# Performance work log

Measured on AMD Instinct MI355X. Metric: run time of the kernel, lower is better.

The kernel has to match this reference:

```python
import jax, jax.numpy as jnp
import numpy as np

B, T, D, E = 2, 1653, 512, 8
D_E = D // E
BE = B * E


def setup_inputs() -> dict:
    key = jax.random.key(0)
    ks = jax.random.split(key, 11)
    s = 0.02  # keep linear-layer scale sane
    return {
        "input": jax.random.normal(ks[0], (B, T, D), jnp.float32),
        "Wq": jax.random.normal(ks[1], (D, D), jnp.float32) * s,
        "bq": jax.random.normal(ks[2], (D,), jnp.float32) * s,
        "Wk": jax.random.normal(ks[3], (D, D), jnp.float32) * s,
        "bk": jax.random.normal(ks[4], (D,), jnp.float32) * s,
        "Wv": jax.random.normal(ks[5], (D, D), jnp.float32) * s,
        "bv": jax.random.normal(ks[6], (D,), jnp.float32) * s,
        "Wo": jax.random.normal(ks[7], (D, D), jnp.float32) * s,
        "bo": jax.random.normal(ks[8], (D,), jnp.float32) * s,
        # random 'gaussian orthogonal punishment' matrix (diag(norms) @ blockwise-QR in torch; random here)
        "punish": jax.random.normal(ks[9], (T, T), jnp.float32) * (1.0 / np.sqrt(T)),
        # random tensor produced by torch.nn.init.orthogonal_(att_score) in the source
        "att_orth": jax.random.normal(ks[10], (BE, T, T), jnp.float32) * (1.0 / np.sqrt(T)),
    }


def _learnable_sigmoid(x):
    return 1.2 / (1.0 + jnp.exp(-1.6 * x))


def reference(input, Wq, bq, Wk, bk, Wv, bv, Wo, bo, punish, att_orth):
    # torch nn.Linear: y = x @ W^T + b
    def proj(W, b):
        # [B,T,D] -> permute(0,2,1) -> [B,D,T] -> reshape to [B*E, T, D_E]
        y = jnp.einsum('btd,ed->bte', input, W) + b
        return y.transpose(0, 2, 1).reshape(BE, T, D_E)

    Q = _learnable_sigmoid(proj(Wq, bq))            # [BE, T, D_E] (mask_q is all-ones => no-op)
    K = _learnable_sigmoid(proj(Wk, bk))            # [BE, T, D_E]
    V = proj(Wv, bv)                                # [BE, T, D_E]

    inv_sqrt_T = 1.0 / jnp.sqrt(jnp.float32(T))
    att = jnp.einsum('btd,bsd->bts', Q, K) * inv_sqrt_T  # [BE, T, T]

    # punishment: elementwise mul by broadcast punish matrix, then matmul with
    # the (transposed) random orthogonal tensor: att = (att * P) @ orth^T
    att = (att * punish[None, :, :]) @ att_orth.transpose(0, 2, 1)  # [BE, T, T]

    att = jnp.where(att == 0.0, jnp.float32(-2e20), att)  # masked_fill(att==0, -2e20)

    out = jnp.einsum('bts,bsd->btd', att, V)        # [BE, T, D_E]
    # permute(0,2,1) -> [BE, D_E, T] -> reshape [B, D, T] -> permute -> [B, T, D]
    out = out.transpose(0, 2, 1).reshape(B, D, T).transpose(0, 2, 1)
    return jnp.einsum('btd,ed->bte', out, Wo) + bo   # [B, T, D]
```

## Files before the change

kernel.cpp:

```cpp
#include <hip/hip_runtime.h>

#define TT 1653
#define DD 512
#define BB 2
#define DE 64
#define BEH 16
#define TTILES 26
#define TPAD 1664
#define SQN 26
#define NJC 4
#define MPSTRIDE TPAD

typedef __attribute__((ext_vector_type(8))) short bf16x8;
typedef __attribute__((ext_vector_type(4))) float f32x4;
typedef float f32x4u  __attribute__((ext_vector_type(4), aligned(4)));

__device__ __forceinline__ short f2bf(float f) {
    union { float f; unsigned u; } v; v.f = f;
    unsigned r = v.u + 0x7fffu + ((v.u >> 16) & 1u);
    return (short)(r >> 16);
}
__device__ __forceinline__ unsigned pack2(float a, float b) {
    return (unsigned)(unsigned short)f2bf(a) | ((unsigned)(unsigned short)f2bf(b) << 16);
}
__device__ __forceinline__ float bf2f(short s) {
    union { unsigned u; float f; } v; v.u = ((unsigned)(unsigned short)s) << 16;
    return v.f;
}

__device__ __forceinline__ void bar_fenced() {
    __builtin_amdgcn_sched_barrier(0);
    __builtin_amdgcn_s_barrier();
    __builtin_amdgcn_sched_barrier(0);
}
__device__ __forceinline__ void lgkm0_bar() {
    asm volatile("s_waitcnt lgkmcnt(0)" ::: "memory");
    __builtin_amdgcn_sched_barrier(0);
    __builtin_amdgcn_s_barrier();
    __builtin_amdgcn_sched_barrier(0);
}

__global__ __launch_bounds__(256) void convp2_kernel(
    const float* __restrict__ P, short* __restrict__ Pbf)
{
    const int g = blockIdx.x * 256 + threadIdx.x;
    const int NG4 = TPAD / 4;
    if (g >= TT * NG4) return;
    const int r = g / NG4, c4 = (g - r * NG4) * 4;
    float p0 = 0.f, p1 = 0.f, p2 = 0.f, p3 = 0.f;
    const float* prow = P + (size_t)r * TT;
    if (c4 + 0 < TT) p0 = prow[c4 + 0];
    if (c4 + 1 < TT) p1 = prow[c4 + 1];
    if (c4 + 2 < TT) p2 = prow[c4 + 2];
    if (c4 + 3 < TT) p3 = prow[c4 + 3];
    uint2 o; o.x = pack2(p0, p1); o.y = pack2(p2, p3);
    *(uint2*)(Pbf + (size_t)r * TPAD + c4) = o;
}

__global__ __launch_bounds__(256) void proj4_kernel(
    const float* __restrict__ X,
    const float* __restrict__ W0, const float* __restrict__ b0,
    const float* __restrict__ W1, const float* __restrict__ b1,
    const float* __restrict__ W2, const float* __restrict__ b2,
    short* __restrict__ Y0, short* __restrict__ Y1, short* __restrict__ Y2)
{
    __shared__ __align__(16) short Wsh[64][72];
    __shared__ __align__(16) short Xs[64][72];

    const int tt = blockIdx.x, dt = blockIdx.y, z = blockIdx.z;
    const int b = z / 3, which = z % 3;
    const float* W    = (which == 0) ? W0 : (which == 1) ? W1 : W2;
    const float* bias = (which == 0) ? b0 : (which == 1) ? b1 : b2;
    short* Y          = (which == 0) ? Y0 : (which == 1) ? Y1 : Y2;

    const int t0 = tt * 64, d0 = dt * 64;
    const float* Xb = X + (size_t)b * TT * DD;

    const int tid  = threadIdx.x;
    const int wave = tid >> 6, lane = tid & 63;
    const int quad = lane >> 4, l16 = lane & 15;
    const int srow = tid >> 2, scg = (tid & 3) * 16;
    const int trow = t0 + srow;
    const int rx = min(trow, TT - 1);

    f32x4 acc[4];
    #pragma unroll
    for (int i = 0; i < 4; ++i) acc[i] = (f32x4){0.f, 0.f, 0.f, 0.f};

    float4 w0, w1, w2, w3, x0, x1, x2, x3;

    auto stage = [&](int k0) {
        const float* wrow = W + (size_t)(d0 + srow) * DD + k0 + scg;
        w0 = *(const float4*)(wrow);
        w1 = *(const float4*)(wrow + 4);
        w2 = *(const float4*)(wrow + 8);
        w3 = *(const float4*)(wrow + 12);
        const float* xrow = Xb + (size_t)rx * DD + k0 + scg;
        x0 = *(const float4*)(xrow);
        x1 = *(const float4*)(xrow + 4);
        x2 = *(const float4*)(xrow + 8);
        x3 = *(const float4*)(xrow + 12);
    };
    auto lds_write = [&]() {
        const bool tv = (trow < TT);
        float4 zz = make_float4(0.f, 0.f, 0.f, 0.f);
        float4 y0 = tv ? x0 : zz, y1 = tv ? x1 : zz;
        float4 y2 = tv ? x2 : zz, y3 = tv ? x3 : zz;
        uint4 pw0, pw1, px0, px1;
        pw0.x = pack2(w0.x, w0.y); pw0.y = pack2(w0.z, w0.w);
        pw0.z = pack2(w1.x, w1.y); pw0.w = pack2(w1.z, w1.w);
        pw1.x = pack2(w2.x, w2.y); pw1.y = pack2(w2.z, w2.w);
        pw1.z = pack2(w3.x, w3.y); pw1.w = pack2(w3.z, w3.w);
        px0.x = pack2(y0.x, y0.y); px0.y = pack2(y0.z, y0.w);
        px0.z = pack2(y1.x, y1.y); px0.w = pack2(y1.z, y1.w);
        px1.x = pack2(y2.x, y2.y); px1.y = pack2(y2.z, y2.w);
        px1.z = pack2(y3.x, y3.y); px1.w = pack2(y3.z, y3.w);
        *(uint4*)&Wsh[srow][scg]     = pw0;
        *(uint4*)&Wsh[srow][scg + 8] = pw1;
        *(uint4*)&Xs[srow][scg]      = px0;
        *(uint4*)&Xs[srow][scg + 8]  = px1;
    };

    stage(0);
    for (int k0 = 0; k0 < DD; k0 += 64) {
        lds_write();
        if (k0 + 64 < DD) stage(k0 + 64);
        lgkm0_bar();

        #pragma unroll
        for (int ks = 0; ks < 2; ++ks) {
            bf16x8 a = *(const bf16x8*)&Wsh[wave * 16 + l16][ks * 32 + quad * 8];
            #pragma unroll
            for (int nt = 0; nt < 4; ++nt) {
                bf16x8 bb = *(const bf16x8*)&Xs[nt * 16 + l16][ks * 32 + quad * 8];
                acc[nt] = __builtin_amdgcn_mfma_f32_16x16x32_bf16(a, bb, acc[nt], 0, 0, 0);
            }
        }
        bar_fenced();
    }

    #pragma unroll
    for (int nt = 0; nt < 4; ++nt) {
        const int t = t0 + nt * 16 + l16;
        if (t < TT) {
            #pragma unroll
            for (int r = 0; r < 4; ++r) {
                const int d = d0 + wave * 16 + quad * 4 + r;
                float v = acc[nt][r] + bias[d];
                if (which < 2) v = 1.2f / (1.0f + __expf(-1.6f * v));
                Y[((size_t)b * DD + d) * TT + t] = f2bf(v);
            }
        }
    }
}

struct OVStage {
    f32x4u o0a, o0b, o1a, o1b;
    uint2  v0a, v0b, v1a, v1b;
};

__global__ __launch_bounds__(256) void ovt6_kernel(
    const float* __restrict__ orth, const short* __restrict__ Vb,
    float* __restrict__ Mpart)
{
    __shared__ __align__(16) short Os[64][72];
    __shared__ __align__(16) short Vs[64][72];

    const int sq = blockIdx.x, be = blockIdx.y, jc = blockIdx.z;
    const int s0 = sq * 64;
    const int jt0 = (jc < 2) ? jc * 7 : 14 + (jc - 2) * 6;
    const int jtn = (jc < 2) ? 7 : 6;

    const float* O  = orth + (size_t)be * TT * TT;
    const short* Vh = Vb + (size_t)be * DE * TT;

    const int tid  = threadIdx.x;
    const int wave = tid >> 6, lane = tid & 63;
    const int quad = lane >> 4, l16 = lane & 15;

    const int p  = tid & 15;
    const int sc = tid >> 4;
    const int ca = s0 + 4 * sc;
    const bool fastS = (s0 + 64 <= TT);

    f32x4 acc[4];
    #pragma unroll
    for (int i = 0; i < 4; ++i) acc[i] = (f32x4){0.f, 0.f, 0.f, 0.f};

    auto stage_load = [&](OVStage& S, int j0) {
        const int jA = j0 + 2 * p;
        const int r0  = min(jA,      TT - 1);
        const int r0b = min(jA + 1,  TT - 1);
        const int r1  = min(jA + 32, TT - 1);
        const int r1b = min(jA + 33, TT - 1);
        if (fastS) {
            S.o0a = *(const f32x4u*)(O + (size_t)r0  * TT + ca);
            S.o0b = *(const f32x4u*)(O + (size_t)r0b * TT + ca);
            S.o1a = *(const f32x4u*)(O + (size_t)r1  * TT + ca);
            S.o1b = *(const f32x4u*)(O + (size_t)r1b * TT + ca);
        } else {
            #pragma unroll
            for (int i = 0; i < 4; ++i) {
                const int col = ca + i;
                const bool cv = (col < TT);
                S.o0a[i] = cv ? O[(size_t)r0  * TT + col] : 0.f;
                S.o0b[i] = cv ? O[(size_t)r0b * TT + col] : 0.f;
                S.o1a[i] = cv ? O[(size_t)r1  * TT + col] : 0.f;
                S.o1b[i] = cv ? O[(size_t)r1b * TT + col] : 0.f;
            }
        }
        S.v0a = *(const uint2*)(Vh + (size_t)r0  * DE + 4 * sc);
        S.v0b = *(const uint2*)(Vh + (size_t)r0b * DE + 4 * sc);
        S.v1a = *(const uint2*)(Vh + (size_t)r1  * DE + 4 * sc);
        S.v1b = *(const uint2*)(Vh + (size_t)r1b * DE + 4 * sc);
    };

    auto lds_write = [&](const OVStage& S, int j0) {
        const int jA = j0 + 2 * p;
        #pragma unroll
        for (int i = 0; i < 4; ++i) {
            *(unsigned*)&Os[4 * sc + i][2 * p]      = pack2(S.o0a[i], S.o0b[i]);
            *(unsigned*)&Os[4 * sc + i][2 * p + 32] = pack2(S.o1a[i], S.o1b[i]);
        }
        const uint2 z = make_uint2(0u, 0u);
        uint2 v0a = (jA      < TT) ? S.v0a : z;
        uint2 v0b = (jA + 1  < TT) ? S.v0b : z;
        uint2 v1a = (jA + 32 < TT) ? S.v1a : z;
        uint2 v1b = (jA + 33 < TT) ? S.v1b : z;
        *(unsigned*)&Vs[4 * sc + 0][2 * p]      = (v0a.x & 0xffffu) | (v0b.x << 16);
        *(unsigned*)&Vs[4 * sc + 1][2 * p]      = (v0a.x >> 16)     | (v0b.x & 0xffff0000u);
        *(unsigned*)&Vs[4 * sc + 2][2 * p]      = (v0a.y & 0xffffu) | (v0b.y << 16);
        *(unsigned*)&Vs[4 * sc + 3][2 * p]      = (v0a.y >> 16)     | (v0b.y & 0xffff0000u);
        *(unsigned*)&Vs[4 * sc + 0][2 * p + 32] = (v1a.x & 0xffffu) | (v1b.x << 16);
        *(unsigned*)&Vs[4 * sc + 1][2 * p + 32] = (v1a.x >> 16)     | (v1b.x & 0xffff0000u);
        *(unsigned*)&Vs[4 * sc + 2][2 * p + 32] = (v1a.y & 0xffffu) | (v1b.y << 16);
        *(unsigned*)&Vs[4 * sc + 3][2 * p + 32] = (v1a.y >> 16)     | (v1b.y & 0xffff0000u);
    };

    auto mfma_tile = [&]() {
        #pragma unroll
        for (int ks = 0; ks < 2; ++ks) {
            bf16x8 bb = *(const bf16x8*)&Os[wave * 16 + l16][ks * 32 + quad * 8];
            #pragma unroll
            for (int i = 0; i < 4; ++i) {
                bf16x8 a = *(const bf16x8*)&Vs[i * 16 + l16][ks * 32 + quad * 8];
                acc[i] = __builtin_amdgcn_mfma_f32_16x16x32_bf16(a, bb, acc[i], 0, 0, 0);
            }
        }
    };

    OVStage sA, sB;
    stage_load(sA, (jt0 + 0) * 64);
    stage_load(sB, (jt0 + 1) * 64);

    for (int t = 0; t < jtn; t += 2) {
        lds_write(sA, (jt0 + t) * 64);
        if (t + 2 < jtn) stage_load(sA, (jt0 + t + 2) * 64);
        lgkm0_bar();
        mfma_tile();
        bar_fenced();
        if (t + 1 < jtn) {
            lds_write(sB, (jt0 + t + 1) * 64);
            if (t + 3 < jtn) stage_load(sB, (jt0 + t + 3) * 64);
            lgkm0_bar();
            mfma_tile();
            bar_fenced();
        }
    }

    float* Mp = Mpart + (size_t)(jc * BEH + be) * DE * MPSTRIDE;
    const int s = s0 + wave * 16 + l16;
    #pragma unroll
    for (int i = 0; i < 4; ++i) {
        #pragma unroll
        for (int r = 0; r < 4; ++r) {
            const int d = i * 16 + quad * 4 + r;
            Mp[(size_t)d * MPSTRIDE + s] = acc[i][r];
        }
    }
}

__global__ __launch_bounds__(256) void mreduce_kernel(
    const float* __restrict__ Mpart, short* __restrict__ Mt)
{
    const int g = blockIdx.x * 256 + threadIdx.x;
    const int NG = TPAD / 4;
    if (g >= BEH * DE * NG) return;
    const int bd = g / NG;
    const int s4 = (g - bd * NG) * 4;

    const size_t jstride = (size_t)BEH * DE * MPSTRIDE;
    const float* p = Mpart + (size_t)bd * MPSTRIDE + s4;
    float4 a0 = *(const float4*)(p);
    float4 a1 = *(const float4*)(p + jstride);
    float4 a2 = *(const float4*)(p + 2 * jstride);
    float4 a3 = *(const float4*)(p + 3 * jstride);
    float s0 = a0.x + a1.x + a2.x + a3.x;
    float s1 = a0.y + a1.y + a2.y + a3.y;
    float s2 = a0.z + a1.z + a2.z + a3.z;
    float s3 = a0.w + a1.w + a2.w + a3.w;

    uint2 o;
    o.x = pack2(s0, s1);
    o.y = pack2(s2, s3);
    *(uint2*)(Mt + (size_t)bd * TPAD + s4) = o;
}

struct AStage {
    uint4 k0, k1, m0, m1, p0, p1;
};

__global__ __launch_bounds__(256) void attn4_kernel(
    const short* __restrict__ Qb, const short* __restrict__ Kb,
    const short* __restrict__ Mt, const short* __restrict__ Pbf,
    float* __restrict__ Hbuf)
{
    __shared__ __align__(16) short Qs[64][72];
    __shared__ __align__(16) short Ks[64][72];
    __shared__ __align__(16) short Ms[64][72];
    __shared__ __align__(16) short Ps[64][72];

    const int it = blockIdx.x, be = blockIdx.y;
    const int b = be >> 3, e = be & 7;
    const int i0 = it * 64;
    const short* Qh = Qb + (size_t)be * DE * TT;
    const short* Kh = Kb + (size_t)be * DE * TT;
    const short* Mh = Mt + (size_t)be * DE * TPAD;

    const int tid  = threadIdx.x;
    const int wave = tid >> 6, lane = tid & 63;
    const int quad = lane >> 4, l16 = lane & 15;

    const float invs = 0.024598297f;

    const int srow = tid >> 2, scg = (tid & 3) * 16;
    const int gi = i0 + srow;
    const bool giv = (gi < TT);
    const int ri = min(gi, TT - 1);

    {
        uint4 z = make_uint4(0u, 0u, 0u, 0u);
        uint4 v0 = *(const uint4*)(Qh + (size_t)ri * DE + scg);
        uint4 v1 = *(const uint4*)(Qh + (size_t)ri * DE + scg + 8);
        if (!giv) { v0 = z; v1 = z; }
        *(uint4*)&Qs[srow][scg]     = v0;
        *(uint4*)&Qs[srow][scg + 8] = v1;
    }

    f32x4 out[4];
    #pragma unroll
    for (int i = 0; i < 4; ++i) out[i] = (f32x4){0.f, 0.f, 0.f, 0.f};

    auto stage_regs = [&](AStage& S, int s0) {
        const int gs = s0 + srow;
        const int rs = min(gs, TT - 1);
        S.k0 = *(const uint4*)(Kh + (size_t)rs * DE + scg);
        S.k1 = *(const uint4*)(Kh + (size_t)rs * DE + scg + 8);
        S.m0 = *(const uint4*)(Mh + (size_t)srow * TPAD + s0 + scg);
        S.m1 = *(const uint4*)(Mh + (size_t)srow * TPAD + s0 + scg + 8);
        S.p0 = *(const uint4*)(Pbf + (size_t)ri * TPAD + s0 + scg);
        S.p1 = *(const uint4*)(Pbf + (size_t)ri * TPAD + s0 + scg + 8);
    };

    auto lds_write = [&](const AStage& S, int s0) {
        const int gs = s0 + srow;
        const uint4 z = make_uint4(0u, 0u, 0u, 0u);
        const bool kv = (gs < TT);
        uint4 k0 = kv ? S.k0 : z, k1 = kv ? S.k1 : z;
        uint4 p0 = giv ? S.p0 : z, p1 = giv ? S.p1 : z;
        *(uint4*)&Ks[srow][scg]     = k0;
        *(uint4*)&Ks[srow][scg + 8] = k1;
        *(uint4*)&Ms[srow][scg]     = S.m0;
        *(uint4*)&Ms[srow][scg + 8] = S.m1;
        *(uint4*)&Ps[srow][scg]     = p0;
        *(uint4*)&Ps[srow][scg + 8] = p1;
    };

    auto compute = [&]() {
        f32x4 w[4];
        #pragma unroll
        for (int i = 0; i < 4; ++i) w[i] = (f32x4){0.f, 0.f, 0.f, 0.f};
        #pragma unroll
        for (int ks = 0; ks < 2; ++ks) {
            bf16x8 a = *(const bf16x8*)&Qs[wave * 16 + l16][ks * 32 + quad * 8];
            #pragma unroll
            for (int stile = 0; stile < 4; ++stile) {
                bf16x8 bb = *(const bf16x8*)&Ks[stile * 16 + l16][ks * 32 + quad * 8];
                w[stile] = __builtin_amdgcn_mfma_f32_16x16x32_bf16(a, bb, w[stile], 0, 0, 0);
            }
        }

        #pragma unroll
        for (int stile = 0; stile < 4; ++stile) {
            const int sl = stile * 16 + l16;
            #pragma unroll
            for (int r = 0; r < 4; ++r) {
                const int il = wave * 16 + quad * 4 + r;
                float v = w[stile][r] * invs * bf2f(Ps[il][sl]);
                Ps[il][sl] = f2bf(v);
            }
        }

        #pragma unroll
        for (int ks = 0; ks < 2; ++ks) {
            bf16x8 a = *(const bf16x8*)&Ps[wave * 16 + l16][ks * 32 + quad * 8];
            #pragma unroll
            for (int dt = 0; dt < 4; ++dt) {
                bf16x8 bb = *(const bf16x8*)&Ms[dt * 16 + l16][ks * 32 + quad * 8];
                out[dt] = __builtin_amdgcn_mfma_f32_16x16x32_bf16(a, bb, out[dt], 0, 0, 0);
            }
        }
    };

    AStage sA, sB;
    stage_regs(sA, 0);
    stage_regs(sB, 64);
    lgkm0_bar();

    for (int tt = 0; tt < TTILES; tt += 2) {
        lds_write(sA, tt * 64);
        if (tt + 2 < TTILES) stage_regs(sA, (tt + 2) * 64);
        lgkm0_bar();
        compute();
        bar_fenced();
        lds_write(sB, (tt + 1) * 64);
        if (tt + 3 < TTILES) stage_regs(sB, (tt + 3) * 64);
        lgkm0_bar();
        compute();
        bar_fenced();
    }

    #pragma unroll
    for (int dt = 0; dt < 4; ++dt) {
        const int d = dt * 16 + l16;
        #pragma unroll
        for (int r = 0; r < 4; ++r) {
            const int go = i0 + wave * 16 + quad * 4 + r;
            if (go < TT)
                Hbuf[((size_t)b * TT + go) * DD + e * 64 + d] = out[dt][r];
        }
    }
}

__global__ __launch_bounds__(256) void oproj_kernel(
    const float* __restrict__ H, const float* __restrict__ Wo,
    const float* __restrict__ bo, float* __restrict__ out)
{
    __shared__ float Hs[16][68];
    __shared__ float Ns[16][68];

    const int tt = blockIdx.x, nt = blockIdx.y, b = blockIdx.z;
    const int t0 = tt * 64, n0 = nt * 64;
    const float* Hb = H + (size_t)b * TT * DD;

    const int tid = threadIdx.x;
    const int tx = tid & 15, ty = tid >> 4;
    const int lrow = tid >> 2, lq = tid & 3;
    const int trow = t0 + lrow;

    float acc[4][4] = {};

    for (int k0 = 0; k0 < DD; k0 += 16) {
        float4 hv = make_float4(0.f, 0.f, 0.f, 0.f);
        if (trow < TT)
            hv = *(const float4*)(Hb + (size_t)trow * DD + k0 + lq*4);
        float4 wv = *(const float4*)(Wo + (size_t)(n0 + lrow) * DD + k0 + lq*4);
        __syncthreads();
        Hs[lq*4+0][lrow] = hv.x; Hs[lq*4+1][lrow] = hv.y;
        Hs[lq*4+2][lrow] = hv.z; Hs[lq*4+3][lrow] = hv.w;
        Ns[lq*4+0][lrow] = wv.x; Ns[lq*4+1][lrow] = wv.y;
        Ns[lq*4+2][lrow] = wv.z; Ns[lq*4+3][lrow] = wv.w;
        __syncthreads();
        #pragma unroll
        for (int k = 0; k < 16; ++k) {
            float4 a4 = *(const float4*)(&Hs[k][ty*4]);
            float4 c4 = *(const float4*)(&Ns[k][tx*4]);
            float a[4] = {a4.x, a4.y, a4.z, a4.w};
            float c[4] = {c4.x, c4.y, c4.z, c4.w};
            #pragma unroll
            for (int i = 0; i < 4; ++i)
                #pragma unroll
                for (int j = 0; j < 4; ++j)
                    acc[i][j] = fmaf(a[i], c[j], acc[i][j]);
        }
        __syncthreads();
    }

    #pragma unroll
    for (int i = 0; i < 4; ++i) {
        const int t = t0 + ty*4 + i;
        if (t < TT) {
            float4 v;
            v.x = acc[i][0] + bo[n0 + tx*4 + 0];
            v.y = acc[i][1] + bo[n0 + tx*4 + 1];
            v.z = acc[i][2] + bo[n0 + tx*4 + 2];
            v.w = acc[i][3] + bo[n0 + tx*4 + 3];
            *(float4*)(out + ((size_t)b * TT + t) * DD + n0 + tx*4) = v;
        }
    }
}

extern "C" void kernel_launch(void* const* d_in, const int* in_sizes, int n_in,
                              void* d_out, int out_size, void* d_ws, size_t ws_size,
                              hipStream_t stream)
{
    (void)in_sizes; (void)n_in; (void)out_size; (void)ws_size;

    const float* X    = (const float*)d_in[0];
    const float* Wq   = (const float*)d_in[1];
    const float* bq   = (const float*)d_in[2];
    const float* Wk   = (const float*)d_in[3];
    const float* bk   = (const float*)d_in[4];
    const float* Wv   = (const float*)d_in[5];
    const float* bv   = (const float*)d_in[6];
    const float* Wo   = (const float*)d_in[7];
    const float* bo   = (const float*)d_in[8];
    const float* P    = (const float*)d_in[9];
    const float* orth = (const float*)d_in[10];
    float* out = (float*)d_out;

    char* ws = (char*)d_ws;
    const size_t SZH = (size_t)BB * DD * TT * sizeof(short);
    short* Qb  = (short*)(ws);
    short* Kb  = (short*)(ws + SZH);
    short* Vb  = (short*)(ws + 2 * SZH);
    short* Mtb = (short*)(ws + 3 * SZH);
    short* Pbf = (short*)(ws + 3 * SZH + (size_t)BEH * DE * TPAD * sizeof(short));
    char*  after_p = ws + 3 * SZH + (size_t)BEH * DE * TPAD * sizeof(short)
                        + (size_t)TT * TPAD * sizeof(short);
    float* Mpart = (float*)after_p;
    float* Hbuf  = (float*)after_p;

    dim3 blk(256);

    convp2_kernel<<<dim3((TT * (TPAD / 4) + 255) / 256), blk, 0, stream>>>(P, Pbf);

    dim3 g1(TTILES, DD / 64, BB * 3);
    proj4_kernel<<<g1, blk, 0, stream>>>(X, Wq, bq, Wk, bk, Wv, bv, Qb, Kb, Vb);

    dim3 g2(SQN, BEH, NJC);
    ovt6_kernel<<<g2, blk, 0, stream>>>(orth, Vb, Mpart);

    dim3 gr((BEH * DE * (TPAD / 4) + 255) / 256);
    mreduce_kernel<<<gr, blk, 0, stream>>>(Mpart, Mtb);

    dim3 g3(TTILES, BEH);
    attn4_kernel<<<g3, blk, 0, stream>>>(Qb, Kb, Mtb, Pbf, Hbuf);

    dim3 g4(TTILES, DD / 64, BB);
    oproj_kernel<<<g4, blk, 0, stream>>>(Hbuf, Wo, bo, out);
}
```

Baseline: 406.5 us.

## Fuse punish conversion into projection, add XCD-aware block remap, pad LDS tiles

Folds the punish-matrix bf16 conversion into the projection kernel as an extra grid slice, removing one launch. Remaps block indices in the orth·V and attention kernels so blocks sharing the same head land on the same XCD, aiming for better L2 reuse. Changes LDS row padding from 72 to 70 shorts with 4-byte-aligned fragment loads, and swaps the thread-to-(p,sc) mapping in the orth loader to alter coalescing and bank conflicts. The 70-short padding forces split LDS reads, which may cost more instructions.

```diff
diff --git a/kernel.cpp b/kernel.cpp
--- a/kernel.cpp
+++ b/kernel.cpp
@@ -13,6 +13,7 @@
 
 typedef __attribute__((ext_vector_type(8))) short bf16x8;
 typedef __attribute__((ext_vector_type(4))) float f32x4;
+typedef short bf16x8u __attribute__((ext_vector_type(8), aligned(4)));
 typedef float f32x4u  __attribute__((ext_vector_type(4), aligned(4)));
 
 __device__ __forceinline__ short f2bf(float f) {
@@ -26,6 +27,10 @@
 __device__ __forceinline__ float bf2f(short s) {
     union { unsigned u; float f; } v; v.u = ((unsigned)(unsigned short)s) << 16;
     return v.f;
+}
+__device__ __forceinline__ bf16x8 ld_frag4(const short* p) {
+    bf16x8u v = *(const bf16x8u*)p;
+    return (bf16x8)v;
 }
 
 __device__ __forceinline__ void bar_fenced() {
@@ -40,34 +45,39 @@
     __builtin_amdgcn_sched_barrier(0);
 }
 
-__global__ __launch_bounds__(256) void convp2_kernel(
-    const float* __restrict__ P, short* __restrict__ Pbf)
-{
-    const int g = blockIdx.x * 256 + threadIdx.x;
-    const int NG4 = TPAD / 4;
-    if (g >= TT * NG4) return;
-    const int r = g / NG4, c4 = (g - r * NG4) * 4;
-    float p0 = 0.f, p1 = 0.f, p2 = 0.f, p3 = 0.f;
-    const float* prow = P + (size_t)r * TT;
-    if (c4 + 0 < TT) p0 = prow[c4 + 0];
-    if (c4 + 1 < TT) p1 = prow[c4 + 1];
-    if (c4 + 2 < TT) p2 = prow[c4 + 2];
-    if (c4 + 3 < TT) p3 = prow[c4 + 3];
-    uint2 o; o.x = pack2(p0, p1); o.y = pack2(p2, p3);
-    *(uint2*)(Pbf + (size_t)r * TPAD + c4) = o;
-}
-
-__global__ __launch_bounds__(256) void proj4_kernel(
+__global__ __launch_bounds__(256) void projconv_kernel(
     const float* __restrict__ X,
     const float* __restrict__ W0, const float* __restrict__ b0,
     const float* __restrict__ W1, const float* __restrict__ b1,
     const float* __restrict__ W2, const float* __restrict__ b2,
-    short* __restrict__ Y0, short* __restrict__ Y1, short* __restrict__ Y2)
+    const float* __restrict__ P,
+    short* __restrict__ Y0, short* __restrict__ Y1, short* __restrict__ Y2,
+    short* __restrict__ Pbf)
 {
     __shared__ __align__(16) short Wsh[64][72];
     __shared__ __align__(16) short Xs[64][72];
 
-    const int tt = blockIdx.x, dt = blockIdx.y, z = blockIdx.z;
+    const int tid = threadIdx.x;
+    const int z = blockIdx.z;
+
+    if (z == 6) {
+        const int cid = blockIdx.x + TTILES * blockIdx.y;
+        const int NG4 = TPAD / 4;
+        for (int g = cid * 256 + tid; g < TT * NG4; g += 208 * 256) {
+            const int r = g / NG4, c4 = (g - r * NG4) * 4;
+            float p0 = 0.f, p1 = 0.f, p2 = 0.f, p3 = 0.f;
+            const float* prow = P + (size_t)r * TT;
+            if (c4 + 0 < TT) p0 = prow[c4 + 0];
+            if (c4 + 1 < TT) p1 = prow[c4 + 1];
+            if (c4 + 2 < TT) p2 = prow[c4 + 2];
+            if (c4 + 3 < TT) p3 = prow[c4 + 3];
+            uint2 o; o.x = pack2(p0, p1); o.y = pack2(p2, p3);
+            *(uint2*)(Pbf + (size_t)r * TPAD + c4) = o;
+        }
+        return;
+    }
+
+    const int tt = blockIdx.x, dt = blockIdx.y;
     const int b = z / 3, which = z % 3;
     const float* W    = (which == 0) ? W0 : (which == 1) ? W1 : W2;
     const float* bias = (which == 0) ? b0 : (which == 1) ? b1 : b2;
@@ -76,7 +86,6 @@
     const int t0 = tt * 64, d0 = dt * 64;
     const float* Xb = X + (size_t)b * TT * DD;
 
-    const int tid  = threadIdx.x;
     const int wave = tid >> 6, lane = tid & 63;
     const int quad = lane >> 4, l16 = lane & 15;
     const int srow = tid >> 2, scg = (tid & 3) * 16;
@@ -159,14 +168,21 @@
     uint2  v0a, v0b, v1a, v1b;
 };
 
-__global__ __launch_bounds__(256) void ovt6_kernel(
+__global__ __launch_bounds__(256) void ovt8_kernel(
     const float* __restrict__ orth, const short* __restrict__ Vb,
     float* __restrict__ Mpart)
 {
-    __shared__ __align__(16) short Os[64][72];
-    __shared__ __align__(16) short Vs[64][72];
-
-    const int sq = blockIdx.x, be = blockIdx.y, jc = blockIdx.z;
+    __shared__ __align__(16) short Os[64][70];
+    __shared__ __align__(16) short Vs[64][70];
+
+    const int flat = blockIdx.x + TTILES * (blockIdx.y + BEH * blockIdx.z);
+    const int xcd = flat & 7;
+    const int j8  = flat >> 3;
+    const int sq  = j8 % 26;
+    const int slice = xcd * 8 + (j8 / 26);
+    const int be = slice & 15;
+    const int jc = slice >> 4;
+
     const int s0 = sq * 64;
     const int jt0 = (jc < 2) ? jc * 7 : 14 + (jc - 2) * 6;
     const int jtn = (jc < 2) ? 7 : 6;
@@ -178,8 +194,8 @@
     const int wave = tid >> 6, lane = tid & 63;
     const int quad = lane >> 4, l16 = lane & 15;
 
-    const int p  = tid & 15;
-    const int sc = tid >> 4;
+    const int p  = tid >> 4;
+    const int sc = tid & 15;
     const int ca = s0 + 4 * sc;
     const bool fastS = (s0 + 64 <= TT);
 
@@ -240,10 +256,10 @@
     auto mfma_tile = [&]() {
         #pragma unroll
         for (int ks = 0; ks < 2; ++ks) {
-            bf16x8 bb = *(const bf16x8*)&Os[wave * 16 + l16][ks * 32 + quad * 8];
+            bf16x8 bb = ld_frag4(&Os[wave * 16 + l16][ks * 32 + quad * 8]);
             #pragma unroll
             for (int i = 0; i < 4; ++i) {
-                bf16x8 a = *(const bf16x8*)&Vs[i * 16 + l16][ks * 32 + quad * 8];
+                bf16x8 a = ld_frag4(&Vs[i * 16 + l16][ks * 32 + quad * 8]);
                 acc[i] = __builtin_amdgcn_mfma_f32_16x16x32_bf16(a, bb, acc[i], 0, 0, 0);
             }
         }
@@ -310,7 +326,7 @@
     uint4 k0, k1, m0, m1, p0, p1;
 };
 
-__global__ __launch_bounds__(256) void attn4_kernel(
+__global__ __launch_bounds__(256) void attn6_kernel(
     const short* __restrict__ Qb, const short* __restrict__ Kb,
     const short* __restrict__ Mt, const short* __restrict__ Pbf,
     float* __restrict__ Hbuf)
@@ -320,7 +336,12 @@
     __shared__ __align__(16) short Ms[64][72];
     __shared__ __align__(16) short Ps[64][72];
 
-    const int it = blockIdx.x, be = blockIdx.y;
+    const int flat = blockIdx.x + TTILES * blockIdx.y;
+    const int xcd = flat & 7;
+    const int j8  = flat >> 3;
+    const int it  = j8 % 26;
+    const int be  = xcd * 2 + (j8 / 26);
+
     const int b = be >> 3, e = be & 7;
     const int i0 = it * 64;
     const short* Qh = Qb + (size_t)be * DE * TT;
@@ -533,19 +554,18 @@
 
     dim3 blk(256);
 
-    convp2_kernel<<<dim3((TT * (TPAD / 4) + 255) / 256), blk, 0, stream>>>(P, Pbf);
-
-    dim3 g1(TTILES, DD / 64, BB * 3);
-    proj4_kernel<<<g1, blk, 0, stream>>>(X, Wq, bq, Wk, bk, Wv, bv, Qb, Kb, Vb);
+    dim3 g1(TTILES, DD / 64, BB * 3 + 1);
+    projconv_kernel<<<g1, blk, 0, stream>>>(X, Wq, bq, Wk, bk, Wv, bv, P,
+                                            Qb, Kb, Vb, Pbf);
 
     dim3 g2(SQN, BEH, NJC);
-    ovt6_kernel<<<g2, blk, 0, stream>>>(orth, Vb, Mpart);
+    ovt8_kernel<<<g2, blk, 0, stream>>>(orth, Vb, Mpart);
 
     dim3 gr((BEH * DE * (TPAD / 4) + 255) / 256);
     mreduce_kernel<<<gr, blk, 0, stream>>>(Mpart, Mtb);
 
     dim3 g3(TTILES, BEH);
-    attn4_kernel<<<g3, blk, 0, stream>>>(Qb, Kb, Mtb, Pbf, Hbuf);
+    attn6_kernel<<<g3, blk, 0, stream>>>(Qb, Kb, Mtb, Pbf, Hbuf);
 
     dim3 g4(TTILES, DD / 64, BB);
     oproj_kernel<<<g4, blk, 0, stream>>>(Hbuf, Wo, bo, out);
```

After: 408.3 us. About the same (+0.4%).
